# Optimization experiments

Hardware: AMD Instinct MI355X
Metric: run time of the kernel (lower is better)

## Reference

```python
import jax, jax.numpy as jnp
import numpy as np

B, H, S, D = 2, 16, 2048, 64
SOFTCLAMP = 50.0


def setup_inputs() -> dict:
    key = jax.random.key(0)
    kq, kk, kv, km = jax.random.split(key, 4)
    q = jax.random.normal(kq, (B, H, S, D), dtype=jnp.float32)
    k = jax.random.normal(kk, (B, H, S, D), dtype=jnp.float32)
    v = jax.random.normal(kv, (B, H, S, D), dtype=jnp.float32)
    mask = jax.random.randint(km, (B, S), 0, 2).astype(jnp.bool_)
    return {"q": q, "k": k, "v": v, "mask": mask}


def reference(q, k, v, mask):
    scale = q.shape[-1] ** -0.5
    # [b, h, i, j] similarity logits
    sim = jnp.einsum('bhid,bhjd->bhij', q, k) * scale
    # tanh-based logit softclamping (Gemma2-style softcapping)
    sim = jnp.tanh(sim / SOFTCLAMP) * SOFTCLAMP
    mask_value = -jnp.finfo(sim.dtype).max
    sim = jnp.where(mask[:, None, None, :], sim, mask_value)
    attn = jax.nn.softmax(sim, axis=-1)
    out = jnp.einsum('bhij,bhjd->bhid', attn, v)
    return out, attn
```

## Files before the change

kernel.cpp:

```cpp
#include <hip/hip_runtime.h>
#include <hip/hip_bf16.h>

#define B_ 2
#define H_ 16
#define S_ 2048
#define D_ 64
#define PSTR 2056

typedef float f32x4 __attribute__((ext_vector_type(4)));
typedef short s16x8 __attribute__((ext_vector_type(8)));
typedef short s16x4 __attribute__((ext_vector_type(4)));

__device__ __forceinline__ short f2bf(float f) {
  unsigned u = __float_as_uint(f);
  u += 0x7FFFu + ((u >> 16) & 1u);
  return (short)(u >> 16);
}
__device__ __forceinline__ float bf2f(short s) {
  return __uint_as_float(((unsigned)(unsigned short)s) << 16);
}

__device__ __forceinline__ float softcap_p(float a) {
  const float k1 = 0.18033688011f;
  const float k2 = -3.7570183e-07f;
  const float k3 = 9.3926761e-13f;
  const float C  = 72.134752044f;
  float y = a * a;
  float t = __builtin_fmaf(y, k3, k2);
  t = __builtin_fmaf(y, t, k1);
  float arg = __builtin_fmaf(a, t, -C);
  arg = fminf(arg, 0.f);
  return exp2f(arg);
}

__global__ __launch_bounds__(256) void prep_qk(const float* __restrict__ q,
                                               const float* __restrict__ k,
                                               short* __restrict__ qbf,
                                               short* __restrict__ kbf) {
  size_t i = ((size_t)blockIdx.x * 256 + threadIdx.x) * 8;
  const f32x4* qa = (const f32x4*)(q + i);
  const f32x4* ka = (const f32x4*)(k + i);
  f32x4 a0 = __builtin_nontemporal_load(qa);
  f32x4 a1 = __builtin_nontemporal_load(qa + 1);
  f32x4 b0 = __builtin_nontemporal_load(ka);
  f32x4 b1 = __builtin_nontemporal_load(ka + 1);
  s16x8 oq, ok;
  #pragma unroll
  for (int e = 0; e < 4; ++e) {
    oq[e] = f2bf(a0[e]); oq[4 + e] = f2bf(a1[e]);
    ok[e] = f2bf(b0[e]); ok[4 + e] = f2bf(b1[e]);
  }
  *(s16x8*)(qbf + i) = oq;
  *(s16x8*)(kbf + i) = ok;
}

__global__ __launch_bounds__(256) void prep_v(const float* __restrict__ v,
                                              short* __restrict__ vt) {
  __shared__ float tile[64][65];
  const int tid = threadIdx.x;
  const int j0 = blockIdx.x * 64;
  const int bh = blockIdx.y;
  const float* vh = v + (size_t)bh * S_ * D_;
  #pragma unroll
  for (int it = 0; it < 16; ++it) {
    int idx = it * 256 + tid;
    int row = idx >> 6, col = idx & 63;
    tile[row][col] = __builtin_nontemporal_load(&vh[(size_t)(j0 + row) * D_ + col]);
  }
  __syncthreads();
  short* vth = vt + (size_t)bh * D_ * S_;
  #pragma unroll
  for (int it = 0; it < 16; ++it) {
    int idx = it * 256 + tid;
    int d = idx >> 6, jj = idx & 63;
    vth[(size_t)d * S_ + j0 + jj] = f2bf(tile[jj][d]);
  }
}

template <bool PRE>
__global__ __launch_bounds__(512, 2) void attend_fused(
    const float* __restrict__ q, const float* __restrict__ k,
    const float* __restrict__ v, const int* __restrict__ mask,
    const short* __restrict__ qbf, const short* __restrict__ kbf,
    const short* __restrict__ vt,
    float* __restrict__ out, float* __restrict__ attn) {
  __shared__ short strip[16 * PSTR];
  __shared__ float ls_rs[8][16];
  __shared__ float ls_rinv[16];

  const int tid  = threadIdx.x;
  const int wv   = tid >> 6;
  const int lane = tid & 63;
  const int lg   = lane >> 4;
  const int li   = lane & 15;

  const unsigned flat = blockIdx.y * gridDim.x + blockIdx.x;
  const unsigned swz  = (flat & 7) * 512 + (flat >> 3);
  const int q0 = (int)(swz & 127) * 16;
  const int bh = (int)(swz >> 7);
  const int b  = bh >> 4;
  const int* mrow = mask + (size_t)b * S_;

  s16x8 qf0, qf1;
  if constexpr (PRE) {
    const short* qr = qbf + ((size_t)bh * S_ + q0 + li) * D_ + lg * 8;
    qf0 = *(const s16x8*)qr;
    qf1 = *(const s16x8*)(qr + 32);
  } else {
    const float* qr = q + ((size_t)bh * S_ + q0 + li) * D_ + lg * 8;
    #pragma unroll
    for (int e = 0; e < 8; ++e) { qf0[e] = f2bf(qr[e]); qf1[e] = f2bf(qr[32 + e]); }
  }

  const short* kbase = PRE ? (kbf + (size_t)bh * S_ * D_) : nullptr;
  s16x8 kf[8];
  auto ldK = [&](int cc) {
    const int jcc = cc * 512 + wv * 64;
    #pragma unroll
    for (int n = 0; n < 4; ++n) {
      const short* kr = kbase + (size_t)(jcc + n * 16 + li) * D_ + lg * 8;
      kf[2 * n]     = *(const s16x8*)kr;
      kf[2 * n + 1] = *(const s16x8*)(kr + 32);
    }
  };
  if constexpr (PRE) ldK(0);

  float rs[4] = {0.f, 0.f, 0.f, 0.f};
  f32x4 pvacc[4];
  #pragma unroll
  for (int m = 0; m < 4; ++m) pvacc[m] = (f32x4){0.f, 0.f, 0.f, 0.f};

  #pragma unroll
  for (int c = 0; c < 4; ++c) {
    const int jc = c * 512 + wv * 64;

    f32x4 acc[4];
    #pragma unroll
    for (int n = 0; n < 4; ++n) acc[n] = (f32x4){0.f, 0.f, 0.f, 0.f};
    if constexpr (PRE) {
      #pragma unroll
      for (int n = 0; n < 4; ++n) {
        acc[n] = __builtin_amdgcn_mfma_f32_16x16x32_bf16(qf0, kf[2 * n], acc[n], 0, 0, 0);
        acc[n] = __builtin_amdgcn_mfma_f32_16x16x32_bf16(qf1, kf[2 * n + 1], acc[n], 0, 0, 0);
      }
      if (c < 3) ldK(c + 1);
    } else {
      #pragma unroll
      for (int n = 0; n < 4; ++n) {
        const float* kr = k + ((size_t)bh * S_ + jc + n * 16 + li) * D_ + lg * 8;
        s16x8 k0, k1;
        #pragma unroll
        for (int e = 0; e < 8; ++e) { k0[e] = f2bf(kr[e]); k1[e] = f2bf(kr[32 + e]); }
        acc[n] = __builtin_amdgcn_mfma_f32_16x16x32_bf16(qf0, k0, acc[n], 0, 0, 0);
        acc[n] = __builtin_amdgcn_mfma_f32_16x16x32_bf16(qf1, k1, acc[n], 0, 0, 0);
      }
    }

    #pragma unroll
    for (int n = 0; n < 4; ++n) {
      const int j = jc + n * 16 + li;
      const bool keep = mrow[j] != 0;
      #pragma unroll
      for (int r = 0; r < 4; ++r) {
        float pp = softcap_p(acc[n][r]);
        float pv_ = keep ? pp : 0.f;
        rs[r] += pv_;
        strip[(lg * 4 + r) * PSTR + j] = f2bf(pv_);
      }
    }

    #pragma unroll
    for (int ks = 0; ks < 2; ++ks) {
      s16x8 pa = *(const s16x8*)&strip[li * PSTR + jc + ks * 32 + lg * 8];
      #pragma unroll
      for (int m = 0; m < 4; ++m) {
        s16x8 vb;
        if constexpr (PRE) {
          vb = *(const s16x8*)(vt + ((size_t)bh * D_ + m * 16 + li) * S_ + jc + ks * 32 + lg * 8);
        } else {
          const float* vp = v + (size_t)bh * S_ * D_ + (size_t)(jc + ks * 32 + lg * 8) * D_ + m * 16 + li;
          #pragma unroll
          for (int e = 0; e < 8; ++e) vb[e] = f2bf(vp[(size_t)e * D_]);
        }
        pvacc[m] = __builtin_amdgcn_mfma_f32_16x16x32_bf16(pa, vb, pvacc[m], 0, 0, 0);
      }
    }
  }

  #pragma unroll
  for (int r = 0; r < 4; ++r) {
    #pragma unroll
    for (int m = 1; m < 16; m <<= 1) rs[r] += __shfl_xor(rs[r], m, 64);
  }
  if (li == 0) {
    #pragma unroll
    for (int r = 0; r < 4; ++r) ls_rs[wv][lg * 4 + r] = rs[r];
  }
  __syncthreads();
  if (tid < 16) {
    float ssum = 0.f;
    #pragma unroll
    for (int w = 0; w < 8; ++w) ssum += ls_rs[w][tid];
    ls_rinv[tid] = (ssum > 0.f) ? 1.f / ssum : 0.f;
  }
  __syncthreads();

  float* abase = attn + ((size_t)bh * S_ + q0) * S_;
  #pragma unroll
  for (int rr = 0; rr < 2; ++rr) {
    const int row = wv * 2 + rr;
    const float rv = ls_rinv[row];
    const short* srow = &strip[row * PSTR];
    float* arow = abase + (size_t)row * S_;
    #pragma unroll
    for (int it = 0; it < 8; ++it) {
      s16x4 pb = *(const s16x4*)&srow[it * 256 + lane * 4];
      f32x4 a;
      a[0] = bf2f(pb[0]) * rv; a[1] = bf2f(pb[1]) * rv;
      a[2] = bf2f(pb[2]) * rv; a[3] = bf2f(pb[3]) * rv;
      *(f32x4*)(arow + it * 256 + lane * 4) = a;
    }
  }

  __syncthreads();

  float (*pvred)[16][64] = (float (*)[16][64])strip;
  #pragma unroll
  for (int m = 0; m < 4; ++m)
    #pragma unroll
    for (int r = 0; r < 4; ++r)
      pvred[wv][lg * 4 + r][m * 16 + li] = pvacc[m][r];
  __syncthreads();

  #pragma unroll
  for (int h = 0; h < 2; ++h) {
    const int idx = h * 512 + tid;
    const int qq = idx >> 6, d = idx & 63;
    float ssum = 0.f;
    #pragma unroll
    for (int w = 0; w < 8; ++w) ssum += pvred[w][qq][d];
    out[((size_t)bh * S_ + q0 + qq) * D_ + d] = ssum * ls_rinv[qq];
  }
}

extern "C" void kernel_launch(void* const* d_in, const int* in_sizes, int n_in,
                              void* d_out, int out_size, void* d_ws, size_t ws_size,
                              hipStream_t stream) {
  const float* q = (const float*)d_in[0];
  const float* k = (const float*)d_in[1];
  const float* v = (const float*)d_in[2];
  const int* mask = (const int*)d_in[3];

  float* out  = (float*)d_out;
  const size_t nel = (size_t)B_ * H_ * S_ * D_;
  float* attn = out + nel;

  dim3 grid(S_ / 16, B_ * H_);
  const size_t need = nel * 2 * 3;

  if (ws_size >= need) {
    short* qbf = (short*)d_ws;
    short* kbf = qbf + nel;
    short* vtp = kbf + nel;
    prep_qk<<<(int)(nel / (256 * 8)), 256, 0, stream>>>(q, k, qbf, kbf);
    prep_v<<<dim3(S_ / 64, B_ * H_), 256, 0, stream>>>(v, vtp);
    attend_fused<true><<<grid, 512, 0, stream>>>(q, k, v, mask, qbf, kbf, vtp, out, attn);
  } else {
    attend_fused<false><<<grid, 512, 0, stream>>>(q, k, v, mask, nullptr, nullptr, nullptr, out, attn);
  }
}
```

Measured before the change: 317.9 us.

## Merge K/V prep kernels, drop Q prep, prefetch V fragments, batch attn stores

Folds the K conversion and the V transpose into one launch and stops pre-converting Q, since each block converts its own Q rows directly from fp32. V fragments are prefetched into registers one chunk ahead, the same way K already was. The clamp before exp2 is removed in favour of the raw hardware exp2 intrinsic, and the attn write-out now loads both rows from LDS before storing. These changes cut launch overhead and workspace traffic and hide V load latency, at the cost of more VGPRs at 512 threads with two blocks per SM.

```diff
diff --git a/kernel.cpp b/kernel.cpp
--- a/kernel.cpp
+++ b/kernel.cpp
@@ -29,51 +29,44 @@
   float t = __builtin_fmaf(y, k3, k2);
   t = __builtin_fmaf(y, t, k1);
   float arg = __builtin_fmaf(a, t, -C);
-  arg = fminf(arg, 0.f);
-  return exp2f(arg);
-}
-
-__global__ __launch_bounds__(256) void prep_qk(const float* __restrict__ q,
-                                               const float* __restrict__ k,
-                                               short* __restrict__ qbf,
-                                               short* __restrict__ kbf) {
-  size_t i = ((size_t)blockIdx.x * 256 + threadIdx.x) * 8;
-  const f32x4* qa = (const f32x4*)(q + i);
-  const f32x4* ka = (const f32x4*)(k + i);
-  f32x4 a0 = __builtin_nontemporal_load(qa);
-  f32x4 a1 = __builtin_nontemporal_load(qa + 1);
-  f32x4 b0 = __builtin_nontemporal_load(ka);
-  f32x4 b1 = __builtin_nontemporal_load(ka + 1);
-  s16x8 oq, ok;
-  #pragma unroll
-  for (int e = 0; e < 4; ++e) {
-    oq[e] = f2bf(a0[e]); oq[4 + e] = f2bf(a1[e]);
-    ok[e] = f2bf(b0[e]); ok[4 + e] = f2bf(b1[e]);
-  }
-  *(s16x8*)(qbf + i) = oq;
-  *(s16x8*)(kbf + i) = ok;
-}
-
-__global__ __launch_bounds__(256) void prep_v(const float* __restrict__ v,
-                                              short* __restrict__ vt) {
-  __shared__ float tile[64][65];
-  const int tid = threadIdx.x;
-  const int j0 = blockIdx.x * 64;
-  const int bh = blockIdx.y;
-  const float* vh = v + (size_t)bh * S_ * D_;
-  #pragma unroll
-  for (int it = 0; it < 16; ++it) {
-    int idx = it * 256 + tid;
-    int row = idx >> 6, col = idx & 63;
-    tile[row][col] = __builtin_nontemporal_load(&vh[(size_t)(j0 + row) * D_ + col]);
-  }
-  __syncthreads();
-  short* vth = vt + (size_t)bh * D_ * S_;
-  #pragma unroll
-  for (int it = 0; it < 16; ++it) {
-    int idx = it * 256 + tid;
-    int d = idx >> 6, jj = idx & 63;
-    vth[(size_t)d * S_ + j0 + jj] = f2bf(tile[jj][d]);
+  return __builtin_amdgcn_exp2f(arg);
+}
+
+#define KBLK ((B_ * H_ * S_ * D_) / (256 * 8))
+__global__ __launch_bounds__(256) void prep_kv(const float* __restrict__ k,
+                                               const float* __restrict__ v,
+                                               short* __restrict__ kbf,
+                                               short* __restrict__ vt) {
+  if ((int)blockIdx.x < KBLK) {
+    size_t i = ((size_t)blockIdx.x * 256 + threadIdx.x) * 8;
+    const f32x4* ka = (const f32x4*)(k + i);
+    f32x4 b0 = __builtin_nontemporal_load(ka);
+    f32x4 b1 = __builtin_nontemporal_load(ka + 1);
+    s16x8 ok;
+    #pragma unroll
+    for (int e = 0; e < 4; ++e) { ok[e] = f2bf(b0[e]); ok[4 + e] = f2bf(b1[e]); }
+    *(s16x8*)(kbf + i) = ok;
+  } else {
+    __shared__ float tile[64][65];
+    const int blk = (int)blockIdx.x - KBLK;
+    const int j0 = (blk & 31) * 64;
+    const int bh = blk >> 5;
+    const int tid = threadIdx.x;
+    const float* vh = v + (size_t)bh * S_ * D_;
+    #pragma unroll
+    for (int it = 0; it < 16; ++it) {
+      int idx = it * 256 + tid;
+      int row = idx >> 6, col = idx & 63;
+      tile[row][col] = __builtin_nontemporal_load(&vh[(size_t)(j0 + row) * D_ + col]);
+    }
+    __syncthreads();
+    short* vth = vt + (size_t)bh * D_ * S_;
+    #pragma unroll
+    for (int it = 0; it < 16; ++it) {
+      int idx = it * 256 + tid;
+      int d = idx >> 6, jj = idx & 63;
+      vth[(size_t)d * S_ + j0 + jj] = f2bf(tile[jj][d]);
+    }
   }
 }
 
@@ -81,8 +74,7 @@
 __global__ __launch_bounds__(512, 2) void attend_fused(
     const float* __restrict__ q, const float* __restrict__ k,
     const float* __restrict__ v, const int* __restrict__ mask,
-    const short* __restrict__ qbf, const short* __restrict__ kbf,
-    const short* __restrict__ vt,
+    const short* __restrict__ kbf, const short* __restrict__ vt,
     float* __restrict__ out, float* __restrict__ attn) {
   __shared__ short strip[16 * PSTR];
   __shared__ float ls_rs[8][16];
@@ -102,18 +94,15 @@
   const int* mrow = mask + (size_t)b * S_;
 
   s16x8 qf0, qf1;
-  if constexpr (PRE) {
-    const short* qr = qbf + ((size_t)bh * S_ + q0 + li) * D_ + lg * 8;
-    qf0 = *(const s16x8*)qr;
-    qf1 = *(const s16x8*)(qr + 32);
-  } else {
+  {
     const float* qr = q + ((size_t)bh * S_ + q0 + li) * D_ + lg * 8;
     #pragma unroll
     for (int e = 0; e < 8; ++e) { qf0[e] = f2bf(qr[e]); qf1[e] = f2bf(qr[32 + e]); }
   }
 
   const short* kbase = PRE ? (kbf + (size_t)bh * S_ * D_) : nullptr;
-  s16x8 kf[8];
+  const short* vbase = PRE ? (vt + (size_t)bh * D_ * S_) : nullptr;
+  s16x8 kf[8], vf[8];
   auto ldK = [&](int cc) {
     const int jcc = cc * 512 + wv * 64;
     #pragma unroll
@@ -123,7 +112,16 @@
       kf[2 * n + 1] = *(const s16x8*)(kr + 32);
     }
   };
-  if constexpr (PRE) ldK(0);
+  auto ldV = [&](int cc) {
+    const int jcc = cc * 512 + wv * 64;
+    #pragma unroll
+    for (int m = 0; m < 4; ++m) {
+      const short* vr = vbase + (size_t)(m * 16 + li) * S_ + jcc + lg * 8;
+      vf[2 * m]     = *(const s16x8*)vr;
+      vf[2 * m + 1] = *(const s16x8*)(vr + 32);
+    }
+  };
+  if constexpr (PRE) { ldK(0); ldV(0); }
 
   float rs[4] = {0.f, 0.f, 0.f, 0.f};
   f32x4 pvacc[4];
@@ -172,19 +170,22 @@
     #pragma unroll
     for (int ks = 0; ks < 2; ++ks) {
       s16x8 pa = *(const s16x8*)&strip[li * PSTR + jc + ks * 32 + lg * 8];
-      #pragma unroll
-      for (int m = 0; m < 4; ++m) {
-        s16x8 vb;
-        if constexpr (PRE) {
-          vb = *(const s16x8*)(vt + ((size_t)bh * D_ + m * 16 + li) * S_ + jc + ks * 32 + lg * 8);
-        } else {
+      if constexpr (PRE) {
+        #pragma unroll
+        for (int m = 0; m < 4; ++m)
+          pvacc[m] = __builtin_amdgcn_mfma_f32_16x16x32_bf16(pa, vf[2 * m + ks], pvacc[m], 0, 0, 0);
+      } else {
+        #pragma unroll
+        for (int m = 0; m < 4; ++m) {
+          s16x8 vb;
           const float* vp = v + (size_t)bh * S_ * D_ + (size_t)(jc + ks * 32 + lg * 8) * D_ + m * 16 + li;
           #pragma unroll
           for (int e = 0; e < 8; ++e) vb[e] = f2bf(vp[(size_t)e * D_]);
+          pvacc[m] = __builtin_amdgcn_mfma_f32_16x16x32_bf16(pa, vb, pvacc[m], 0, 0, 0);
         }
-        pvacc[m] = __builtin_amdgcn_mfma_f32_16x16x32_bf16(pa, vb, pvacc[m], 0, 0, 0);
-      }
-    }
+      }
+    }
+    if constexpr (PRE) { if (c < 3) ldV(c + 1); }
   }
 
   #pragma unroll
@@ -205,20 +206,28 @@
   }
   __syncthreads();
 
-  float* abase = attn + ((size_t)bh * S_ + q0) * S_;
-  #pragma unroll
-  for (int rr = 0; rr < 2; ++rr) {
-    const int row = wv * 2 + rr;
-    const float rv = ls_rinv[row];
-    const short* srow = &strip[row * PSTR];
-    float* arow = abase + (size_t)row * S_;
+  {
+    const int row0 = wv * 2, row1 = wv * 2 + 1;
+    const float rv0 = ls_rinv[row0], rv1 = ls_rinv[row1];
+    s16x4 pb0[8], pb1[8];
     #pragma unroll
     for (int it = 0; it < 8; ++it) {
-      s16x4 pb = *(const s16x4*)&srow[it * 256 + lane * 4];
-      f32x4 a;
-      a[0] = bf2f(pb[0]) * rv; a[1] = bf2f(pb[1]) * rv;
-      a[2] = bf2f(pb[2]) * rv; a[3] = bf2f(pb[3]) * rv;
-      *(f32x4*)(arow + it * 256 + lane * 4) = a;
+      pb0[it] = *(const s16x4*)&strip[row0 * PSTR + it * 256 + lane * 4];
+      pb1[it] = *(const s16x4*)&strip[row1 * PSTR + it * 256 + lane * 4];
+    }
+    float* abase = attn + ((size_t)bh * S_ + q0) * S_;
+    float* arow0 = abase + (size_t)row0 * S_;
+    float* arow1 = abase + (size_t)row1 * S_;
+    #pragma unroll
+    for (int it = 0; it < 8; ++it) {
+      f32x4 a0, a1;
+      #pragma unroll
+      for (int e = 0; e < 4; ++e) {
+        a0[e] = bf2f(pb0[it][e]) * rv0;
+        a1[e] = bf2f(pb1[it][e]) * rv1;
+      }
+      *(f32x4*)(arow0 + it * 256 + lane * 4) = a0;
+      *(f32x4*)(arow1 + it * 256 + lane * 4) = a1;
     }
   }
 
@@ -256,16 +265,14 @@
   float* attn = out + nel;
 
   dim3 grid(S_ / 16, B_ * H_);
-  const size_t need = nel * 2 * 3;
+  const size_t need = nel * 2 * 2;
 
   if (ws_size >= need) {
-    short* qbf = (short*)d_ws;
-    short* kbf = qbf + nel;
+    short* kbf = (short*)d_ws;
     short* vtp = kbf + nel;
-    prep_qk<<<(int)(nel / (256 * 8)), 256, 0, stream>>>(q, k, qbf, kbf);
-    prep_v<<<dim3(S_ / 64, B_ * H_), 256, 0, stream>>>(v, vtp);
-    attend_fused<true><<<grid, 512, 0, stream>>>(q, k, v, mask, qbf, kbf, vtp, out, attn);
+    prep_kv<<<KBLK + 32 * B_ * H_, 256, 0, stream>>>(k, v, kbf, vtp);
+    attend_fused<true><<<grid, 512, 0, stream>>>(q, k, v, mask, kbf, vtp, out, attn);
   } else {
-    attend_fused<false><<<grid, 512, 0, stream>>>(q, k, v, mask, nullptr, nullptr, nullptr, out, attn);
-  }
-}
+    attend_fused<false><<<grid, 512, 0, stream>>>(q, k, v, mask, nullptr, nullptr, out, attn);
+  }
+}
```

Result: slower. 334.6 us (+5.2%).
